# Performance work log

Measured on AMD Instinct MI355X. Metric: run time of the kernel, lower is better.

Reference implementation:

```python
import jax, jax.numpy as jnp
import numpy as np


def setup_inputs() -> dict:
    key = jax.random.key(0)
    k1, k2 = jax.random.split(key)
    B, N, M, D = 8, 8192, 8192, 3
    x = jax.random.normal(k1, (B, N, D), dtype=jnp.float32)
    y = jax.random.normal(k2, (B, M, D), dtype=jnp.float32)
    return {"x": x, "y": y}


def reference(x, y):
    # dist[b, i, j] = |x_bi|^2 + |y_bj|^2 - 2 * <x_bi, y_bj>
    # (same math as the torch code's rx.transpose(2,1) + ry - 2*xy, but
    #  computed with row-norm vectors instead of full NxN / MxM bmms)
    xx = jnp.sum(x * x, axis=-1)                      # [B, N]
    yy = jnp.sum(y * y, axis=-1)                      # [B, M]
    xy = jnp.einsum('bnd,bmd->bnm', x, y)             # [B, N, M]
    dist = xx[:, :, None] + yy[:, None, :] - 2.0 * xy # [B, N, M]
    dist1 = jnp.min(dist, axis=1)  # min over x points -> per-y nearest  [B, M]
    dist2 = jnp.min(dist, axis=2)  # min over y points -> per-x nearest  [B, N]
    return jnp.mean(dist1) + jnp.mean(dist2)
```

## Files before the change

### kernel.cpp

```cpp
#include <hip/hip_runtime.h>


#define B_ 8
#define N_ 8192
#define PTS (B_ * N_)
#define TPB 512

typedef short bf16x8 __attribute__((ext_vector_type(8)));
typedef float f32x16 __attribute__((ext_vector_type(16)));

__device__ __forceinline__ unsigned b16(float f) {
  unsigned u = __float_as_uint(f);
  return (u + 0x7FFFu + ((u >> 16) & 1u)) >> 16;
}
__device__ __forceinline__ float bf(unsigned h) { return __uint_as_float(h << 16); }

__device__ __forceinline__ void build_chunk(const float* __restrict__ cb,
                                            uint4* __restrict__ dst, int t) {
  const unsigned one = 0x3F80u;
#pragma unroll
  for (int q = 0; q < 2; ++q) {
    int p = t + q * TPB;
    float c0 = cb[3 * p], c1 = cb[3 * p + 1], c2 = cb[3 * p + 2];
    float nc = fmaf(c0, c0, fmaf(c1, c1, c2 * c2));
    unsigned yh0 = b16(c0), yh1 = b16(c1), yh2 = b16(c2);
    unsigned yl0 = b16(c0 - bf(yh0)), yl1 = b16(c1 - bf(yh1)), yl2 = b16(c2 - bf(yh2));
    unsigned nh = b16(nc), nl = b16(nc - bf(nh));
    int tt = p >> 5, mm = p & 31;
    dst[tt * 64 + mm]      = make_uint4(yh0 | (yh1 << 16), yh2 | (yl0 << 16),
                                        yl1 | (yl2 << 16), yh0 | (yh1 << 16));
    dst[tt * 64 + 32 + mm] = make_uint4(yh2 | (one << 16), one | (nh << 16),
                                        nl, 0u);
  }
}

__global__ __launch_bounds__(TPB, 4) void chamfer_k(
    const float* __restrict__ x, const float* __restrict__ y,
    float* __restrict__ out) {
  __shared__ uint4 ldsFrag[2][32 * 64];
  __shared__ float red[8];

  const unsigned one = 0x3F80u;
  int t = threadIdx.x, lane = t & 63, w = t >> 6;
  int b = blockIdx.x;
  int dir = b >> 8;
  int bb = b & 255;
  int batch = bb >> 5;
  int rowSeg = bb & 31;
  const float* __restrict__ own  = dir ? y : x;
  const float* __restrict__ cand = dir ? x : y;

  int m = lane & 31;
  int row0 = batch * N_ + rowSeg * 256 + w * 32;
  const float* po = own + 3 * (row0 + m);
  float v0 = po[0], v1 = po[1], v2 = po[2];
  float nv = fmaf(v0, v0, fmaf(v1, v1, v2 * v2));
  float a0 = -2.0f * v0, a1 = -2.0f * v1, a2 = -2.0f * v2;
  unsigned ah0 = b16(a0), ah1 = b16(a1), ah2 = b16(a2);
  unsigned al0 = b16(a0 - bf(ah0)), al1 = b16(a1 - bf(ah1)), al2 = b16(a2 - bf(ah2));
  unsigned nh = b16(nv), nl = b16(nv - bf(nh));
  uint4 h0 = make_uint4(ah0 | (ah1 << 16), ah2 | (ah0 << 16),
                        ah1 | (ah2 << 16), al0 | (al1 << 16));
  uint4 h1 = make_uint4(al2 | (nh << 16), nl | (one << 16), one, 0u);
  uint4 afr;
  afr.x = (lane < 32) ? h0.x : h1.x;
  afr.y = (lane < 32) ? h0.y : h1.y;
  afr.z = (lane < 32) ? h0.z : h1.z;
  afr.w = (lane < 32) ? h0.w : h1.w;
  bf16x8 A = __builtin_bit_cast(bf16x8, afr);

  f32x16 z = {0.f,0.f,0.f,0.f,0.f,0.f,0.f,0.f,0.f,0.f,0.f,0.f,0.f,0.f,0.f,0.f};
  f32x16 rmA, rmB;
#pragma unroll
  for (int r = 0; r < 16; ++r) { rmA[r] = 1e30f; rmB[r] = 1e30f; }

  const float* cbb = cand + batch * N_ * 3;
  build_chunk(cbb, ldsFrag[0], t);
  __syncthreads();

  for (int ch = 0; ch < 8; ++ch) {
    const uint4* cur = ldsFrag[ch & 1];
    if (ch < 7)
      build_chunk(cbb + (ch + 1) * 1024 * 3, ldsFrag[(ch + 1) & 1], t);

#pragma unroll 2
    for (int i = 0; i < 8; ++i) {
      bf16x8 B0 = __builtin_bit_cast(bf16x8, cur[(4 * i + 0) * 64 + lane]);
      bf16x8 B1 = __builtin_bit_cast(bf16x8, cur[(4 * i + 1) * 64 + lane]);
      bf16x8 B2 = __builtin_bit_cast(bf16x8, cur[(4 * i + 2) * 64 + lane]);
      bf16x8 B3 = __builtin_bit_cast(bf16x8, cur[(4 * i + 3) * 64 + lane]);
      f32x16 acc0 = __builtin_amdgcn_mfma_f32_32x32x16_bf16(A, B0, z, 0, 0, 0);
      f32x16 acc1 = __builtin_amdgcn_mfma_f32_32x32x16_bf16(A, B1, z, 0, 0, 0);
      f32x16 acc2 = __builtin_amdgcn_mfma_f32_32x32x16_bf16(A, B2, z, 0, 0, 0);
      f32x16 acc3 = __builtin_amdgcn_mfma_f32_32x32x16_bf16(A, B3, z, 0, 0, 0);
#pragma unroll
      for (int r = 0; r < 16; ++r) {
        rmA[r] = fminf(fminf(rmA[r], acc0[r]), acc1[r]);
        rmB[r] = fminf(fminf(rmB[r], acc2[r]), acc3[r]);
      }
    }
    __syncthreads();
  }

#pragma unroll
  for (int r = 0; r < 16; ++r) rmA[r] = fminf(rmA[r], rmB[r]);
#pragma unroll
  for (int msk = 1; msk <= 16; msk <<= 1) {
#pragma unroll
    for (int r = 0; r < 16; ++r)
      rmA[r] = fminf(rmA[r], __shfl_xor(rmA[r], msk, 64));
  }
  float s = 0.0f;
#pragma unroll
  for (int r = 0; r < 16; ++r) s += rmA[r];
  s += __shfl_xor(s, 32, 64);
  if (lane == 0) red[w] = s;
  __syncthreads();
  if (t == 0) {
    float bs = 0.0f;
#pragma unroll
    for (int c = 0; c < 8; ++c) bs += red[c];
    atomicAdd(out, bs * (1.0f / (float)PTS));
  }
}

extern "C" void kernel_launch(void* const* d_in, const int* in_sizes, int n_in,
                              void* d_out, int out_size, void* d_ws, size_t ws_size,
                              hipStream_t stream) {
  const float* x = (const float*)d_in[0];
  const float* y = (const float*)d_in[1];
  float* out = (float*)d_out;
  hipMemsetAsync(out, 0, sizeof(float), stream);
  chamfer_k<<<512, TPB, 0, stream>>>(x, y, out);
}
```

Measured before the change: 95.56 us.

## Register-block four A fragments per wave and split candidates across two blocks

```diff
diff --git a/kernel.cpp b/kernel.cpp
--- a/kernel.cpp
+++ b/kernel.cpp
@@ -34,93 +34,114 @@
   }
 }
 
-__global__ __launch_bounds__(TPB, 4) void chamfer_k(
+__global__ __launch_bounds__(TPB, 2) void chamfer_main_k(
     const float* __restrict__ x, const float* __restrict__ y,
-    float* __restrict__ out) {
+    float* __restrict__ gpart) {
   __shared__ uint4 ldsFrag[2][32 * 64];
-  __shared__ float red[8];
 
   const unsigned one = 0x3F80u;
   int t = threadIdx.x, lane = t & 63, w = t >> 6;
   int b = blockIdx.x;
-  int dir = b >> 8;
-  int bb = b & 255;
-  int batch = bb >> 5;
-  int rowSeg = bb & 31;
+  int g = b >> 1;
+  int hf = b & 1;
+  int dir = g >> 6;
+  int gg = g & 63;
+  int batch = gg >> 3;
+  int seg = gg & 7;
   const float* __restrict__ own  = dir ? y : x;
   const float* __restrict__ cand = dir ? x : y;
 
   int m = lane & 31;
-  int row0 = batch * N_ + rowSeg * 256 + w * 32;
-  const float* po = own + 3 * (row0 + m);
-  float v0 = po[0], v1 = po[1], v2 = po[2];
-  float nv = fmaf(v0, v0, fmaf(v1, v1, v2 * v2));
-  float a0 = -2.0f * v0, a1 = -2.0f * v1, a2 = -2.0f * v2;
-  unsigned ah0 = b16(a0), ah1 = b16(a1), ah2 = b16(a2);
-  unsigned al0 = b16(a0 - bf(ah0)), al1 = b16(a1 - bf(ah1)), al2 = b16(a2 - bf(ah2));
-  unsigned nh = b16(nv), nl = b16(nv - bf(nh));
-  uint4 h0 = make_uint4(ah0 | (ah1 << 16), ah2 | (ah0 << 16),
-                        ah1 | (ah2 << 16), al0 | (al1 << 16));
-  uint4 h1 = make_uint4(al2 | (nh << 16), nl | (one << 16), one, 0u);
-  uint4 afr;
-  afr.x = (lane < 32) ? h0.x : h1.x;
-  afr.y = (lane < 32) ? h0.y : h1.y;
-  afr.z = (lane < 32) ? h0.z : h1.z;
-  afr.w = (lane < 32) ? h0.w : h1.w;
-  bf16x8 A = __builtin_bit_cast(bf16x8, afr);
+  int rowBase = batch * N_ + seg * 1024 + w * 128;
+  bf16x8 A[4];
+#pragma unroll
+  for (int a = 0; a < 4; ++a) {
+    const float* po = own + 3 * (rowBase + a * 32 + m);
+    float v0 = po[0], v1 = po[1], v2 = po[2];
+    float nv = fmaf(v0, v0, fmaf(v1, v1, v2 * v2));
+    float a0 = -2.0f * v0, a1 = -2.0f * v1, a2 = -2.0f * v2;
+    unsigned ah0 = b16(a0), ah1 = b16(a1), ah2 = b16(a2);
+    unsigned al0 = b16(a0 - bf(ah0)), al1 = b16(a1 - bf(ah1)), al2 = b16(a2 - bf(ah2));
+    unsigned nh = b16(nv), nl = b16(nv - bf(nh));
+    uint4 h0 = make_uint4(ah0 | (ah1 << 16), ah2 | (ah0 << 16),
+                          ah1 | (ah2 << 16), al0 | (al1 << 16));
+    uint4 h1 = make_uint4(al2 | (nh << 16), nl | (one << 16), one, 0u);
+    uint4 afr;
+    afr.x = (lane < 32) ? h0.x : h1.x;
+    afr.y = (lane < 32) ? h0.y : h1.y;
+    afr.z = (lane < 32) ? h0.z : h1.z;
+    afr.w = (lane < 32) ? h0.w : h1.w;
+    A[a] = __builtin_bit_cast(bf16x8, afr);
+  }
 
   f32x16 z = {0.f,0.f,0.f,0.f,0.f,0.f,0.f,0.f,0.f,0.f,0.f,0.f,0.f,0.f,0.f,0.f};
-  f32x16 rmA, rmB;
+  f32x16 rm[4];
 #pragma unroll
-  for (int r = 0; r < 16; ++r) { rmA[r] = 1e30f; rmB[r] = 1e30f; }
+  for (int a = 0; a < 4; ++a)
+#pragma unroll
+    for (int r = 0; r < 16; ++r) rm[a][r] = 1e30f;
 
-  const float* cbb = cand + batch * N_ * 3;
+  const float* cbb = cand + (batch * N_ + hf * 4096) * 3;
   build_chunk(cbb, ldsFrag[0], t);
   __syncthreads();
 
-  for (int ch = 0; ch < 8; ++ch) {
+  for (int ch = 0; ch < 4; ++ch) {
     const uint4* cur = ldsFrag[ch & 1];
-    if (ch < 7)
+    if (ch < 3)
       build_chunk(cbb + (ch + 1) * 1024 * 3, ldsFrag[(ch + 1) & 1], t);
 
-#pragma unroll 2
-    for (int i = 0; i < 8; ++i) {
-      bf16x8 B0 = __builtin_bit_cast(bf16x8, cur[(4 * i + 0) * 64 + lane]);
-      bf16x8 B1 = __builtin_bit_cast(bf16x8, cur[(4 * i + 1) * 64 + lane]);
-      bf16x8 B2 = __builtin_bit_cast(bf16x8, cur[(4 * i + 2) * 64 + lane]);
-      bf16x8 B3 = __builtin_bit_cast(bf16x8, cur[(4 * i + 3) * 64 + lane]);
-      f32x16 acc0 = __builtin_amdgcn_mfma_f32_32x32x16_bf16(A, B0, z, 0, 0, 0);
-      f32x16 acc1 = __builtin_amdgcn_mfma_f32_32x32x16_bf16(A, B1, z, 0, 0, 0);
-      f32x16 acc2 = __builtin_amdgcn_mfma_f32_32x32x16_bf16(A, B2, z, 0, 0, 0);
-      f32x16 acc3 = __builtin_amdgcn_mfma_f32_32x32x16_bf16(A, B3, z, 0, 0, 0);
+    for (int i = 0; i < 16; ++i) {
+      bf16x8 B0 = __builtin_bit_cast(bf16x8, cur[(2 * i) * 64 + lane]);
+      bf16x8 B1 = __builtin_bit_cast(bf16x8, cur[(2 * i + 1) * 64 + lane]);
 #pragma unroll
-      for (int r = 0; r < 16; ++r) {
-        rmA[r] = fminf(fminf(rmA[r], acc0[r]), acc1[r]);
-        rmB[r] = fminf(fminf(rmB[r], acc2[r]), acc3[r]);
+      for (int a = 0; a < 4; ++a) {
+        f32x16 acc0 = __builtin_amdgcn_mfma_f32_32x32x16_bf16(A[a], B0, z, 0, 0, 0);
+        f32x16 acc1 = __builtin_amdgcn_mfma_f32_32x32x16_bf16(A[a], B1, z, 0, 0, 0);
+#pragma unroll
+        for (int r = 0; r < 16; ++r)
+          rm[a][r] = fminf(fminf(rm[a][r], acc0[r]), acc1[r]);
       }
     }
     __syncthreads();
   }
 
 #pragma unroll
-  for (int r = 0; r < 16; ++r) rmA[r] = fminf(rmA[r], rmB[r]);
+  for (int a = 0; a < 4; ++a)
 #pragma unroll
-  for (int msk = 1; msk <= 16; msk <<= 1) {
+    for (int msk = 1; msk <= 16; msk <<= 1)
 #pragma unroll
-    for (int r = 0; r < 16; ++r)
-      rmA[r] = fminf(rmA[r], __shfl_xor(rmA[r], msk, 64));
+      for (int r = 0; r < 16; ++r)
+        rm[a][r] = fminf(rm[a][r], __shfl_xor(rm[a][r], msk, 64));
+
+  float* gp = gpart + b * 1024;
+  if ((lane & 31) == 0) {
+    int h = lane >> 5;
+#pragma unroll
+    for (int a = 0; a < 4; ++a)
+#pragma unroll
+      for (int r = 0; r < 16; ++r)
+        gp[w * 128 + a * 32 + (r & 3) + 8 * (r >> 2) + 4 * h] = rm[a][r];
   }
+}
+
+__global__ __launch_bounds__(256) void chamfer_final_k(
+    const float* __restrict__ gpart, float* __restrict__ out) {
+  int i = blockIdx.x * 256 + threadIdx.x;
   float s = 0.0f;
 #pragma unroll
-  for (int r = 0; r < 16; ++r) s += rmA[r];
-  s += __shfl_xor(s, 32, 64);
-  if (lane == 0) red[w] = s;
+  for (int e = 0; e < 4; ++e) {
+    int rowid = 4 * i + e;
+    int g = rowid >> 10, r = rowid & 1023;
+    s += fminf(gpart[(2 * g) * 1024 + r], gpart[(2 * g + 1) * 1024 + r]);
+  }
+  for (int off = 32; off > 0; off >>= 1) s += __shfl_down(s, off, 64);
+  __shared__ float red[4];
+  int lane = threadIdx.x & 63, wv = threadIdx.x >> 6;
+  if (lane == 0) red[wv] = s;
   __syncthreads();
-  if (t == 0) {
-    float bs = 0.0f;
-#pragma unroll
-    for (int c = 0; c < 8; ++c) bs += red[c];
-    atomicAdd(out, bs * (1.0f / (float)PTS));
+  if (threadIdx.x == 0) {
+    float tt = (red[0] + red[1]) + (red[2] + red[3]);
+    atomicAdd(out, tt * (1.0f / (float)PTS));
   }
 }
 
@@ -130,6 +151,9 @@
   const float* x = (const float*)d_in[0];
   const float* y = (const float*)d_in[1];
   float* out = (float*)d_out;
+  float* gpart = (float*)d_ws;
+
   hipMemsetAsync(out, 0, sizeof(float), stream);
-  chamfer_k<<<512, TPB, 0, stream>>>(x, y, out);
+  chamfer_main_k<<<256, TPB, 0, stream>>>(x, y, gpart);
+  chamfer_final_k<<<128, 256, 0, stream>>>(gpart, out);
 }
```

After: 95.11 us. Within noise of the previous version (-0.5%).
